# Performance work log

Hardware: AMD Instinct MI355X
Metric: run time of the kernel (lower is better)

Reference implementation:

```python
import jax, jax.numpy as jnp
import numpy as np


def setup_inputs() -> dict:
    key = jax.random.key(0)
    ks = jax.random.split(key, 7)
    B, T, I, H, O = 64, 2048, 32, 256, 32
    s = 0.05
    return {
        "x": jax.random.normal(ks[0], (B, T, I), dtype=jnp.float32),
        "W_ih": jax.random.normal(ks[1], (4 * H, I), dtype=jnp.float32) * s,
        "W_hh": jax.random.normal(ks[2], (4 * H, H), dtype=jnp.float32) * s,
        "b_ih": jax.random.normal(ks[3], (4 * H,), dtype=jnp.float32) * s,
        "b_hh": jax.random.normal(ks[4], (4 * H,), dtype=jnp.float32) * s,
        "fc_w": jax.random.normal(ks[5], (O, H), dtype=jnp.float32) * s,
        "fc_b": jax.random.normal(ks[6], (O,), dtype=jnp.float32) * s,
    }


def _lstm(x, W_ih, W_hh, b_ih, b_hh):
    # x: [B,T,I]; PyTorch gate order: i, f, g, o stacked along 4H axis.
    B = x.shape[0]
    H = W_hh.shape[1]
    # Precompute input contributions for all timesteps in one GEMM: [B,T,4H]
    xg = jnp.einsum('bti,gi->btg', x, W_ih) + b_ih + b_hh

    def step(carry, xg_t):
        h, c = carry  # [B,H] each
        gates = xg_t + h @ W_hh.T  # [B,4H]
        i, f, g, o = jnp.split(gates, 4, axis=-1)
        i = jax.nn.sigmoid(i)
        f = jax.nn.sigmoid(f)
        g = jnp.tanh(g)
        o = jax.nn.sigmoid(o)
        c = f * c + i * g
        h = o * jnp.tanh(c)
        return (h, c), h

    h0 = jnp.zeros((B, H), dtype=x.dtype)
    (_, _), hs = jax.lax.scan(step, (h0, h0), jnp.swapaxes(xg, 0, 1))
    return jnp.swapaxes(hs, 0, 1)  # [B,T,H]


def reference(x, W_ih, W_hh, b_ih, b_hh, fc_w, fc_b):
    out = _lstm(x, W_ih, W_hh, b_ih, b_hh)          # [B,T,H]
    # Conv1d(H, O, kernel_size=1) over channel dim == pointwise linear.
    return jnp.einsum('bth,oh->bto', out, fc_w) + fc_b  # [B,T,O]
```

## Files before the change

kernel.cpp:

```cpp
#include <hip/hip_runtime.h>
#include <cstdint>


#define B_  64
#define T_  2048
#define I_  32
#define H_  256
#define O_  32
#define MB  4
#define NBLK 16

typedef int v4i __attribute__((ext_vector_type(4)));
typedef unsigned int v4u __attribute__((ext_vector_type(4)));
typedef float f32x4 __attribute__((ext_vector_type(4)));
typedef _Float16 f16x8 __attribute__((ext_vector_type(8)));
typedef _Float16 h2_t __attribute__((ext_vector_type(2)));

union U16x8 { v4u u; f16x8 h; };

__device__ __forceinline__ float row16_max(float v) {
    int t;
    t = __builtin_amdgcn_update_dpp(__float_as_int(v), __float_as_int(v), 0x111, 0xf, 0xf, false);
    v = fmaxf(v, __int_as_float(t));
    t = __builtin_amdgcn_update_dpp(__float_as_int(v), __float_as_int(v), 0x112, 0xf, 0xf, false);
    v = fmaxf(v, __int_as_float(t));
    t = __builtin_amdgcn_update_dpp(__float_as_int(v), __float_as_int(v), 0x114, 0xf, 0xf, false);
    v = fmaxf(v, __int_as_float(t));
    t = __builtin_amdgcn_update_dpp(__float_as_int(v), __float_as_int(v), 0x118, 0xf, 0xf, false);
    v = fmaxf(v, __int_as_float(t));
    return v;
}

#define WQ_OFF    0
#define S1P_OFF   262144
#define BIASP_OFF 266240
#define WIHH2_OFF 270336
#define FCF_OFF   335872
#define XH_OFF    352256

__device__ __forceinline__ uint32_t pack_q(int q0, int q1, int q2, int q3) {
    return  ((uint32_t)(uint8_t)(int8_t)q0)
          | (((uint32_t)(uint8_t)(int8_t)q1) << 8)
          | (((uint32_t)(uint8_t)(int8_t)q2) << 16)
          | (((uint32_t)(uint8_t)(int8_t)q3) << 24);
}

__device__ __forceinline__ int clamp127(int v) {
    return v < -127 ? -127 : (v > 127 ? 127 : v);
}


__global__ __launch_bounds__(64) void prep_wq(
    const float* __restrict__ Whh, const float* __restrict__ Wih,
    const float* __restrict__ bih, const float* __restrict__ bhh,
    uint32_t* __restrict__ wq2, float* __restrict__ s1p,
    float* __restrict__ biasp, uint32_t* __restrict__ wihh2)
{
    const int gr = blockIdx.x;
    const int j  = threadIdx.x;
    const int g  = gr >> 8, r = gr & 255;
    const int c  = ((r >> 4) << 6) | (g << 4) | (r & 15);

    const float4 wv = ((const float4*)(Whh + gr * H_))[j];
    float m = fmaxf(fmaxf(fabsf(wv.x), fabsf(wv.y)), fmaxf(fabsf(wv.z), fabsf(wv.w)));
    #pragma unroll
    for (int s = 1; s < 64; s <<= 1) m = fmaxf(m, __shfl_xor(m, s, 64));
    const float S1 = fmaxf(m, 1e-20f) / 127.f;
    const float r1 = 1.f / S1;

    wq2[((c >> 4) * 16 + (j >> 2)) * 64 + (c & 15) * 4 + (j & 3)] = pack_q(
        clamp127((int)rintf(wv.x * r1)), clamp127((int)rintf(wv.y * r1)),
        clamp127((int)rintf(wv.z * r1)), clamp127((int)rintf(wv.w * r1)));

    if (j < 16) {
        union { uint32_t u; h2_t h; } z;
        z.h[0] = (_Float16)Wih[gr * I_ + 2 * j];
        z.h[1] = (_Float16)Wih[gr * I_ + 2 * j + 1];
        wihh2[((c >> 4) * 4 + (j >> 2)) * 64 + (c & 15) * 4 + (j & 3)] = z.u;
    }
    if (j == 0) { s1p[c] = S1; biasp[c] = bih[gr] + bhh[gr]; }
}

__global__ __launch_bounds__(256) void prep_xh(
    const float* __restrict__ x, uint32_t* __restrict__ xh)
{
    const int i = blockIdx.x * 256 + threadIdx.x;
    const float2 v = ((const float2*)x)[i];
    union { uint32_t u; h2_t h; } z;
    z.h[0] = (_Float16)v.x; z.h[1] = (_Float16)v.y;
    xh[i] = z.u;
}

__global__ __launch_bounds__(64) void prep_fcf(
    const float* __restrict__ fcw, uint32_t* __restrict__ fcf)
{
    const int id = blockIdx.x * 64 + threadIdx.x;
    const int fw = id >> 9, rem = id & 511;
    const int ks = rem >> 6, l = rem & 63;
    const int o  = fw * 16 + (l & 15);
    const int kb = ks * 32 + (l >> 4) * 8;
    const float* src = fcw + o * H_ + kb;
    #pragma unroll
    for (int e = 0; e < 4; e++) {
        union { uint32_t u; h2_t h; } z;
        z.h[0] = (_Float16)src[2 * e];
        z.h[1] = (_Float16)src[2 * e + 1];
        fcf[id * 4 + e] = z.u;
    }
}

__global__ __launch_bounds__(512, 2) void lstm_mfma(
    const uint32_t* __restrict__ wq2, const float* __restrict__ s1p,
    const float* __restrict__ biasp, const uint32_t* __restrict__ wihh2,
    const uint32_t* __restrict__ xh, const uint32_t* __restrict__ fcf,
    const float* __restrict__ fcb, float* __restrict__ out)
{
    const int blk = blockIdx.x, tid = threadIdx.x;
    const int wvi = tid >> 6, l = tid & 63, lq = l >> 4, lo = l & 15;
    const int b   = lo >> 2;

    __shared__ __align__(16) char     Ab[2][1088];
    __shared__ __align__(16) _Float16 hf[2][1088];
    __shared__ int shmax[2][4];

    v4i  wB[8][4];
    float s1c[8], biasc[8];
    #pragma unroll
    for (int nt = 0; nt < 8; nt++) {
        const int c = wvi * 128 + nt * 16 + lo;
        s1c[nt] = s1p[c]; biasc[nt] = biasp[c];
        #pragma unroll
        for (int kt = 0; kt < 4; kt++)
            wB[nt][kt] = *(const v4i*)(wq2 +
                (size_t)(((wvi * 8 + nt) * 16 + kt * 4 + lq) * 64 + lo * 4));
    }
    const f32x4 fcbv = *(const f32x4*)(fcb + (wvi & 1) * 16 + lq * 4);

    for (int i = tid; i < 1088; i += 512) Ab[1][i] = 0;
    if (tid < 8) ((int*)shmax)[tid] = 0;
    __syncthreads();

    const uint32_t* xrow = xh + ((size_t)(blk * MB + b) * T_) * 16 + lq * 4;
    v4u xA = *(const v4u*)xrow;

    float cst0 = 0.f, cst1 = 0.f;

    for (int t = 0; t < T_; t++) {
        const int rb = (t & 1) ^ 1, cb = t & 1;

        const float spm = __int_as_float(shmax[rb][lq]);

        const v4i af0 = *(const v4i*)&Ab[rb][b * 272 +   0 + lq * 16];
        const v4i af1 = *(const v4i*)&Ab[rb][b * 272 +  64 + lq * 16];
        const v4i af2 = *(const v4i*)&Ab[rb][b * 272 + 128 + lq * 16];
        const v4i af3 = *(const v4i*)&Ab[rb][b * 272 + 192 + lq * 16];

        const int tn = (t + 1 < T_) ? (t + 1) : t;
        const v4u xAn = *(const v4u*)(xrow + (size_t)tn * 16);
        v4u wX[8];
        #pragma unroll
        for (int nt = 0; nt < 8; nt++)
            wX[nt] = *(const v4u*)(wihh2 +
                (size_t)(((wvi * 8 + nt) * 4 + lq) * 64 + lo * 4));

        v4i Ci[8];
        #pragma unroll
        for (int nt = 0; nt < 8; nt++) {
            v4i acc = {0, 0, 0, 0};
            acc = __builtin_amdgcn_mfma_i32_16x16x64_i8(af0, wB[nt][0], acc, 0, 0, 0);
            acc = __builtin_amdgcn_mfma_i32_16x16x64_i8(af1, wB[nt][1], acc, 0, 0, 0);
            acc = __builtin_amdgcn_mfma_i32_16x16x64_i8(af2, wB[nt][2], acc, 0, 0, 0);
            acc = __builtin_amdgcn_mfma_i32_16x16x64_i8(af3, wB[nt][3], acc, 0, 0, 0);
            Ci[nt] = acc;
        }

        if (wvi < 2 && t > 0) {
            f32x4 cfc = {0.f, 0.f, 0.f, 0.f};
            #pragma unroll
            for (int ks = 0; ks < 8; ks++) {
                U16x8 aw, bh;
                aw.u = *(const v4u*)(fcf + (size_t)(((wvi * 8 + ks) * 64 + l) * 4));
                bh.u = *(const v4u*)&hf[rb][b * 272 + ks * 32 + lq * 8];
                cfc = __builtin_amdgcn_mfma_f32_16x16x32_f16(aw.h, bh.h, cfc, 0, 0, 0);
            }
            if ((lo & 3) == 0) {
                const f32x4 r = cfc + fcbv;
                *(f32x4*)(out + ((size_t)(blk * MB + b) * T_ + (t - 1)) * O_
                          + (wvi * 16 + lq * 4)) = r;
            }
        }

        const float sp = spm * (1.f / 127.f);
        float ga[8];
        {
            U16x8 xa; xa.u = xA;
            #pragma unroll
            for (int nt = 0; nt < 8; nt++) {
                const float v = (float)Ci[nt][0] * (s1c[nt] * sp) + biasc[nt];
                f32x4 cf = {v, v, v, v};
                U16x8 wx; wx.u = wX[nt];
                cf = __builtin_amdgcn_mfma_f32_16x16x32_f16(xa.h, wx.h, cf, 0, 0, 0);
                ga[nt] = cf[0];
            }
        }

        const float i0 = 1.f / (1.f + __expf(-ga[0]));
        const float f0 = 1.f / (1.f + __expf(-ga[1]));
        const float g0 = 2.f / (1.f + __expf(-2.f * ga[2])) - 1.f;
        const float o0 = 1.f / (1.f + __expf(-ga[3]));
        cst0 = f0 * cst0 + i0 * g0;
        const float h0 = o0 * (2.f / (1.f + __expf(-2.f * cst0)) - 1.f);

        const float i1 = 1.f / (1.f + __expf(-ga[4]));
        const float f1 = 1.f / (1.f + __expf(-ga[5]));
        const float g1 = 2.f / (1.f + __expf(-2.f * ga[6])) - 1.f;
        const float o1 = 1.f / (1.f + __expf(-ga[7]));
        cst1 = f1 * cst1 + i1 * g1;
        const float h1 = o1 * (2.f / (1.f + __expf(-2.f * cst1)) - 1.f);

        float vm = fmaxf(fabsf(h0), fabsf(h1));
        vm = row16_max(vm);
        if (lo == 15) atomicMax(&shmax[cb][lq], __float_as_int(vm));

        asm volatile("s_waitcnt lgkmcnt(0)" ::: "memory");
        __builtin_amdgcn_s_barrier();

        const float mm = fmaxf(__int_as_float(shmax[cb][lq]), 1e-12f);
        const float rq = 127.f / mm;
        const int r0 = wvi * 32 + lo, r1 = r0 + 16;
        Ab[cb][lq * 272 + r0] = (char)(int8_t)clamp127((int)rintf(h0 * rq));
        Ab[cb][lq * 272 + r1] = (char)(int8_t)clamp127((int)rintf(h1 * rq));
        hf[cb][lq * 272 + r0] = (_Float16)h0;
        hf[cb][lq * 272 + r1] = (_Float16)h1;
        if (tid < 4) shmax[rb][tid] = 0;

        asm volatile("s_waitcnt lgkmcnt(0)" ::: "memory");
        __builtin_amdgcn_s_barrier();

        xA = xAn;
    }

    {
        const int rbF = (T_ - 1) & 1;
        if (wvi < 2) {
            f32x4 cfc = {0.f, 0.f, 0.f, 0.f};
            #pragma unroll
            for (int ks = 0; ks < 8; ks++) {
                U16x8 aw, bh;
                aw.u = *(const v4u*)(fcf + (size_t)(((wvi * 8 + ks) * 64 + l) * 4));
                bh.u = *(const v4u*)&hf[rbF][b * 272 + ks * 32 + lq * 8];
                cfc = __builtin_amdgcn_mfma_f32_16x16x32_f16(aw.h, bh.h, cfc, 0, 0, 0);
            }
            if ((lo & 3) == 0) {
                const f32x4 r = cfc + fcbv;
                *(f32x4*)(out + ((size_t)(blk * MB + b) * T_ + (T_ - 1)) * O_
                          + (wvi * 16 + lq * 4)) = r;
            }
        }
    }
}

extern "C" void kernel_launch(void* const* d_in, const int* in_sizes, int n_in,
                              void* d_out, int out_size, void* d_ws, size_t ws_size,
                              hipStream_t stream) {
    const float* x    = (const float*)d_in[0];
    const float* Wih  = (const float*)d_in[1];
    const float* Whh  = (const float*)d_in[2];
    const float* bih  = (const float*)d_in[3];
    const float* bhh  = (const float*)d_in[4];
    const float* fcw  = (const float*)d_in[5];
    const float* fcb  = (const float*)d_in[6];
    float* out = (float*)d_out;

    char* ws = (char*)d_ws;
    uint32_t* wq2   = (uint32_t*)(ws + WQ_OFF);
    float*    s1p   = (float*)(ws + S1P_OFF);
    float*    biasp = (float*)(ws + BIASP_OFF);
    uint32_t* wihh2 = (uint32_t*)(ws + WIHH2_OFF);
    uint32_t* fcf   = (uint32_t*)(ws + FCF_OFF);
    uint32_t* xh    = (uint32_t*)(ws + XH_OFF);

    prep_wq<<<1024, 64, 0, stream>>>(Whh, Wih, bih, bhh, wq2, s1p, biasp, wihh2);
    prep_xh<<<(B_ * T_ * 16) / 256, 256, 0, stream>>>(x, xh);
    prep_fcf<<<16, 64, 0, stream>>>(fcw, fcf);
    lstm_mfma<<<NBLK, 512, 0, stream>>>(wq2, s1p, biasp, wihh2, xh, fcf, fcb, out);
}
```

Before: 3.704 ms.

## Split recurrent step across 16 waves and batch the FC projection every 4 steps

Doubles the block to 1024 threads so each wave handles 4 gate tiles (one hidden unit per lane) instead of 8, halving the per-wave serial MFMA and activation work on each recurrent step. W_hh int8 tiles are now reloaded from global memory every step instead of being held in registers. The atomicMax scale reduction is replaced by per-wave maxima in shared memory that every lane reduces. The FC projection runs once every 4 steps over a 4-deep fp16 h history ring, which amortises its MFMAs but puts global weight traffic on the critical path each step.

```diff
diff --git a/kernel.cpp b/kernel.cpp
--- a/kernel.cpp
+++ b/kernel.cpp
@@ -95,9 +95,8 @@
     const float* __restrict__ fcw, uint32_t* __restrict__ fcf)
 {
     const int id = blockIdx.x * 64 + threadIdx.x;
-    const int fw = id >> 9, rem = id & 511;
-    const int ks = rem >> 6, l = rem & 63;
-    const int o  = fw * 16 + (l & 15);
+    const int ntile = id >> 9, ks = (id >> 6) & 7, l = id & 63;
+    const int o  = ntile * 16 + (l & 15);
     const int kb = ks * 32 + (l >> 4) * 8;
     const float* src = fcw + o * H_ + kb;
     #pragma unroll
@@ -109,7 +108,7 @@
     }
 }
 
-__global__ __launch_bounds__(512, 2) void lstm_mfma(
+__global__ __launch_bounds__(1024) void lstm_mfma(
     const uint32_t* __restrict__ wq2, const float* __restrict__ s1p,
     const float* __restrict__ biasp, const uint32_t* __restrict__ wihh2,
     const uint32_t* __restrict__ xh, const uint32_t* __restrict__ fcf,
@@ -117,122 +116,107 @@
 {
     const int blk = blockIdx.x, tid = threadIdx.x;
     const int wvi = tid >> 6, l = tid & 63, lq = l >> 4, lo = l & 15;
-    const int b   = lo >> 2;
+    const int xb_ = lo >> 2;
 
     __shared__ __align__(16) char     Ab[2][1088];
-    __shared__ __align__(16) _Float16 hf[2][1088];
-    __shared__ int shmax[2][4];
-
-    v4i  wB[8][4];
-    float s1c[8], biasc[8];
+    __shared__ __align__(16) _Float16 hf[4][1088];
+    __shared__ __align__(16) float    smax[4][16];
+
+    U16x8 wX[4];
+    float s1c[4], biasc[4];
     #pragma unroll
-    for (int nt = 0; nt < 8; nt++) {
-        const int c = wvi * 128 + nt * 16 + lo;
+    for (int nt = 0; nt < 4; nt++) {
+        const int ti = wvi * 4 + nt;
+        const int c  = ti * 16 + lo;
         s1c[nt] = s1p[c]; biasc[nt] = biasp[c];
-        #pragma unroll
-        for (int kt = 0; kt < 4; kt++)
-            wB[nt][kt] = *(const v4i*)(wq2 +
-                (size_t)(((wvi * 8 + nt) * 16 + kt * 4 + lq) * 64 + lo * 4));
-    }
-    const f32x4 fcbv = *(const f32x4*)(fcb + (wvi & 1) * 16 + lq * 4);
-
-    for (int i = tid; i < 1088; i += 512) Ab[1][i] = 0;
-    if (tid < 8) ((int*)shmax)[tid] = 0;
+        wX[nt].u = *(const v4u*)(wihh2 + (size_t)((ti * 4 + lq) * 64 + lo * 4));
+    }
+    const float fb = fcb[(wvi & 1) * 16 + lo];
+
+    if (tid < 272) ((uint32_t*)&Ab[1][0])[tid] = 0;
     __syncthreads();
 
-    const uint32_t* xrow = xh + ((size_t)(blk * MB + b) * T_) * 16 + lq * 4;
+    const uint32_t* xrow = xh + ((size_t)(blk * MB + xb_) * T_) * 16 + lq * 4;
     v4u xA = *(const v4u*)xrow;
 
-    float cst0 = 0.f, cst1 = 0.f;
+    const v4i z4 = {0, 0, 0, 0};
+    float cst = 0.f;
+    float sp  = 0.f;
 
     for (int t = 0; t < T_; t++) {
         const int rb = (t & 1) ^ 1, cb = t & 1;
 
-        const float spm = __int_as_float(shmax[rb][lq]);
-
-        const v4i af0 = *(const v4i*)&Ab[rb][b * 272 +   0 + lq * 16];
-        const v4i af1 = *(const v4i*)&Ab[rb][b * 272 +  64 + lq * 16];
-        const v4i af2 = *(const v4i*)&Ab[rb][b * 272 + 128 + lq * 16];
-        const v4i af3 = *(const v4i*)&Ab[rb][b * 272 + 192 + lq * 16];
+        const v4i af0 = *(const v4i*)&Ab[rb][xb_ * 272 +   0 + lq * 16];
+        const v4i af1 = *(const v4i*)&Ab[rb][xb_ * 272 +  64 + lq * 16];
+        const v4i af2 = *(const v4i*)&Ab[rb][xb_ * 272 + 128 + lq * 16];
+        const v4i af3 = *(const v4i*)&Ab[rb][xb_ * 272 + 192 + lq * 16];
 
         const int tn = (t + 1 < T_) ? (t + 1) : t;
         const v4u xAn = *(const v4u*)(xrow + (size_t)tn * 16);
-        v4u wX[8];
+
+        U16x8 xa; xa.u = xA;
+        float ga[4];
         #pragma unroll
-        for (int nt = 0; nt < 8; nt++)
-            wX[nt] = *(const v4u*)(wihh2 +
-                (size_t)(((wvi * 8 + nt) * 4 + lq) * 64 + lo * 4));
-
-        v4i Ci[8];
-        #pragma unroll
-        for (int nt = 0; nt < 8; nt++) {
-            v4i acc = {0, 0, 0, 0};
-            acc = __builtin_amdgcn_mfma_i32_16x16x64_i8(af0, wB[nt][0], acc, 0, 0, 0);
-            acc = __builtin_amdgcn_mfma_i32_16x16x64_i8(af1, wB[nt][1], acc, 0, 0, 0);
-            acc = __builtin_amdgcn_mfma_i32_16x16x64_i8(af2, wB[nt][2], acc, 0, 0, 0);
-            acc = __builtin_amdgcn_mfma_i32_16x16x64_i8(af3, wB[nt][3], acc, 0, 0, 0);
-            Ci[nt] = acc;
+        for (int nt = 0; nt < 4; nt++) {
+            const int ti = wvi * 4 + nt;
+            const uint32_t* wp = wq2 + (size_t)((ti * 16 + lq) * 64 + lo * 4);
+            const v4i w0 = *(const v4i*)(wp);
+            const v4i w1 = *(const v4i*)(wp + 256);
+            const v4i w2 = *(const v4i*)(wp + 512);
+            const v4i w3 = *(const v4i*)(wp + 768);
+            v4i ci = __builtin_amdgcn_mfma_i32_16x16x64_i8(af0, w0, z4, 0, 0, 0);
+            ci = __builtin_amdgcn_mfma_i32_16x16x64_i8(af1, w1, ci, 0, 0, 0);
+            ci = __builtin_amdgcn_mfma_i32_16x16x64_i8(af2, w2, ci, 0, 0, 0);
+            ci = __builtin_amdgcn_mfma_i32_16x16x64_i8(af3, w3, ci, 0, 0, 0);
+            f32x4 zf = {0.f, 0.f, 0.f, 0.f};
+            const f32x4 cfx = __builtin_amdgcn_mfma_f32_16x16x32_f16(xa.h, wX[nt].h, zf, 0, 0, 0);
+            ga[nt] = cfx[0] + biasc[nt] + (float)ci[0] * (s1c[nt] * sp);
         }
 
-        if (wvi < 2 && t > 0) {
+        if ((t & 3) == 0 && t > 0 && wvi < 2) {
+            const int ts = lo >> 2, fbb = lo & 3;
             f32x4 cfc = {0.f, 0.f, 0.f, 0.f};
             #pragma unroll
             for (int ks = 0; ks < 8; ks++) {
-                U16x8 aw, bh;
-                aw.u = *(const v4u*)(fcf + (size_t)(((wvi * 8 + ks) * 64 + l) * 4));
-                bh.u = *(const v4u*)&hf[rb][b * 272 + ks * 32 + lq * 8];
-                cfc = __builtin_amdgcn_mfma_f32_16x16x32_f16(aw.h, bh.h, cfc, 0, 0, 0);
+                U16x8 aH, bB;
+                aH.u = *(const v4u*)&hf[(t + ts) & 3][fbb * 272 + ks * 32 + lq * 8];
+                bB.u = *(const v4u*)(fcf + (size_t)(((wvi * 8 + ks) * 64 + l) * 4));
+                cfc = __builtin_amdgcn_mfma_f32_16x16x32_f16(aH.h, bB.h, cfc, 0, 0, 0);
             }
-            if ((lo & 3) == 0) {
-                const f32x4 r = cfc + fcbv;
-                *(f32x4*)(out + ((size_t)(blk * MB + b) * T_ + (t - 1)) * O_
-                          + (wvi * 16 + lq * 4)) = r;
-            }
+            #pragma unroll
+            for (int reg = 0; reg < 4; reg++)
+                out[((size_t)(blk * MB + reg) * T_ + (t - 4 + lq)) * O_
+                    + (wvi * 16 + lo)] = cfc[reg] + fb;
         }
 
-        const float sp = spm * (1.f / 127.f);
-        float ga[8];
-        {
-            U16x8 xa; xa.u = xA;
-            #pragma unroll
-            for (int nt = 0; nt < 8; nt++) {
-                const float v = (float)Ci[nt][0] * (s1c[nt] * sp) + biasc[nt];
-                f32x4 cf = {v, v, v, v};
-                U16x8 wx; wx.u = wX[nt];
-                cf = __builtin_amdgcn_mfma_f32_16x16x32_f16(xa.h, wx.h, cf, 0, 0, 0);
-                ga[nt] = cf[0];
-            }
-        }
-
-        const float i0 = 1.f / (1.f + __expf(-ga[0]));
-        const float f0 = 1.f / (1.f + __expf(-ga[1]));
-        const float g0 = 2.f / (1.f + __expf(-2.f * ga[2])) - 1.f;
-        const float o0 = 1.f / (1.f + __expf(-ga[3]));
-        cst0 = f0 * cst0 + i0 * g0;
-        const float h0 = o0 * (2.f / (1.f + __expf(-2.f * cst0)) - 1.f);
-
-        const float i1 = 1.f / (1.f + __expf(-ga[4]));
-        const float f1 = 1.f / (1.f + __expf(-ga[5]));
-        const float g1 = 2.f / (1.f + __expf(-2.f * ga[6])) - 1.f;
-        const float o1 = 1.f / (1.f + __expf(-ga[7]));
-        cst1 = f1 * cst1 + i1 * g1;
-        const float h1 = o1 * (2.f / (1.f + __expf(-2.f * cst1)) - 1.f);
-
-        float vm = fmaxf(fabsf(h0), fabsf(h1));
-        vm = row16_max(vm);
-        if (lo == 15) atomicMax(&shmax[cb][lq], __float_as_int(vm));
+        const float i_ = 1.f / (1.f + __expf(-ga[0]));
+        const float f_ = 1.f / (1.f + __expf(-ga[1]));
+        const float g_ = 2.f / (1.f + __expf(-2.f * ga[2])) - 1.f;
+        const float o_ = 1.f / (1.f + __expf(-ga[3]));
+        cst = f_ * cst + i_ * g_;
+        const float tc = 2.f / (1.f + __expf(-2.f * cst)) - 1.f;
+        const float h = o_ * tc;
+
+        const float vm = row16_max(fabsf(h));
+        if (lo == 15) smax[lq][wvi] = vm;
 
         asm volatile("s_waitcnt lgkmcnt(0)" ::: "memory");
         __builtin_amdgcn_s_barrier();
 
-        const float mm = fmaxf(__int_as_float(shmax[cb][lq]), 1e-12f);
+        const float4 m0 = *(const float4*)&smax[lq][0];
+        const float4 m1 = *(const float4*)&smax[lq][4];
+        const float4 m2 = *(const float4*)&smax[lq][8];
+        const float4 m3 = *(const float4*)&smax[lq][12];
+        float mm = fmaxf(fmaxf(fmaxf(m0.x, m0.y), fmaxf(m0.z, m0.w)),
+                         fmaxf(fmaxf(m1.x, m1.y), fmaxf(m1.z, m1.w)));
+        mm = fmaxf(mm, fmaxf(fmaxf(fmaxf(m2.x, m2.y), fmaxf(m2.z, m2.w)),
+                             fmaxf(fmaxf(m3.x, m3.y), fmaxf(m3.z, m3.w))));
+        mm = fmaxf(mm, 1e-12f);
         const float rq = 127.f / mm;
-        const int r0 = wvi * 32 + lo, r1 = r0 + 16;
-        Ab[cb][lq * 272 + r0] = (char)(int8_t)clamp127((int)rintf(h0 * rq));
-        Ab[cb][lq * 272 + r1] = (char)(int8_t)clamp127((int)rintf(h1 * rq));
-        hf[cb][lq * 272 + r0] = (_Float16)h0;
-        hf[cb][lq * 272 + r1] = (_Float16)h1;
-        if (tid < 4) shmax[rb][tid] = 0;
+        const int r0 = wvi * 16 + lo;
+        Ab[cb][lq * 272 + r0] = (char)(int8_t)clamp127((int)rintf(h * rq));
+        hf[t & 3][lq * 272 + r0] = (_Float16)h;
+        sp = mm * (1.f / 127.f);
 
         asm volatile("s_waitcnt lgkmcnt(0)" ::: "memory");
         __builtin_amdgcn_s_barrier();
@@ -240,23 +224,20 @@
         xA = xAn;
     }
 
-    {
-        const int rbF = (T_ - 1) & 1;
-        if (wvi < 2) {
-            f32x4 cfc = {0.f, 0.f, 0.f, 0.f};
-            #pragma unroll
-            for (int ks = 0; ks < 8; ks++) {
-                U16x8 aw, bh;
-                aw.u = *(const v4u*)(fcf + (size_t)(((wvi * 8 + ks) * 64 + l) * 4));
-                bh.u = *(const v4u*)&hf[rbF][b * 272 + ks * 32 + lq * 8];
-                cfc = __builtin_amdgcn_mfma_f32_16x16x32_f16(aw.h, bh.h, cfc, 0, 0, 0);
-            }
-            if ((lo & 3) == 0) {
-                const f32x4 r = cfc + fcbv;
-                *(f32x4*)(out + ((size_t)(blk * MB + b) * T_ + (T_ - 1)) * O_
-                          + (wvi * 16 + lq * 4)) = r;
-            }
+    if (wvi < 2) {
+        const int ts = lo >> 2, fbb = lo & 3;
+        f32x4 cfc = {0.f, 0.f, 0.f, 0.f};
+        #pragma unroll
+        for (int ks = 0; ks < 8; ks++) {
+            U16x8 aH, bB;
+            aH.u = *(const v4u*)&hf[ts & 3][fbb * 272 + ks * 32 + lq * 8];
+            bB.u = *(const v4u*)(fcf + (size_t)(((wvi * 8 + ks) * 64 + l) * 4));
+            cfc = __builtin_amdgcn_mfma_f32_16x16x32_f16(aH.h, bB.h, cfc, 0, 0, 0);
         }
+        #pragma unroll
+        for (int reg = 0; reg < 4; reg++)
+            out[((size_t)(blk * MB + reg) * T_ + (T_ - 4 + lq)) * O_
+                + (wvi * 16 + lo)] = cfc[reg] + fb;
     }
 }
 
@@ -283,5 +264,5 @@
     prep_wq<<<1024, 64, 0, stream>>>(Whh, Wih, bih, bhh, wq2, s1p, biasp, wihh2);
     prep_xh<<<(B_ * T_ * 16) / 256, 256, 0, stream>>>(x, xh);
     prep_fcf<<<16, 64, 0, stream>>>(fcw, fcf);
-    lstm_mfma<<<NBLK, 512, 0, stream>>>(wq2, s1p, biasp, wihh2, xh, fcf, fcb, out);
-}
+    lstm_mfma<<<NBLK, 1024, 0, stream>>>(wq2, s1p, biasp, wihh2, xh, fcf, fcb, out);
+}
```

New measurement: 5.308 ms. +43.3%, slower.
